# Performance work log

Measured on AMD Instinct MI355X. Metric: run time of the kernel, lower is better.

## Reference

```python
import jax, jax.numpy as jnp
import numpy as np

N_NODES = 100000
N_EDGES = 1600000
N_GRAPHS = 256
F_IN = 54


def setup_inputs() -> dict:
    key = jax.random.key(0)
    ks = jax.random.split(key, 16)
    x = jax.random.normal(ks[0], (N_NODES, F_IN), dtype=jnp.float32)
    edge_index = jax.random.randint(ks[1], (2, N_EDGES), 0, N_NODES, dtype=jnp.int32)
    batch = jnp.sort(jax.random.randint(ks[2], (N_NODES,), 0, N_GRAPHS, dtype=jnp.int32))

    def lin(k, fi, fo):
        kw, kb = jax.random.split(k)
        lim = 1.0 / np.sqrt(fi)
        W = jax.random.uniform(kw, (fi, fo), minval=-lim, maxval=lim, dtype=jnp.float32)
        b = jax.random.uniform(kb, (fo,), minval=-lim, maxval=lim, dtype=jnp.float32)
        return W, b

    W1, b1 = lin(ks[3], 54, 54)
    W2, b2 = lin(ks[4], 54, 108)
    W3, b3 = lin(ks[5], 108, 216)
    Wf1, bf1 = lin(ks[6], 216, 1024)
    Wf2, bf2 = lin(ks[7], 1024, 128)
    return {"x": x, "edge_index": edge_index, "batch": batch,
            "W1": W1, "b1": b1, "W2": W2, "b2": b2, "W3": W3, "b3": b3,
            "Wf1": Wf1, "bf1": bf1, "Wf2": Wf2, "bf2": bf2}


def _gcn_norm(edge_index, n):
    # add self-loops, symmetric degree normalization (PyG GCNConv default)
    loop = jnp.arange(n, dtype=edge_index.dtype)
    row = jnp.concatenate([edge_index[0], loop])
    col = jnp.concatenate([edge_index[1], loop])
    deg = jax.ops.segment_sum(jnp.ones_like(col, dtype=jnp.float32), col, num_segments=n)
    dinv = jnp.where(deg > 0, jax.lax.rsqrt(deg), 0.0)
    norm = dinv[row] * dinv[col]
    return row, col, norm


def _gcn_conv(x, row, col, norm, W, b, n):
    h = x @ W                                  # [N, Fout]
    msg = h[row] * norm[:, None]               # [E+N, Fout] gather + scale
    out = jax.ops.segment_sum(msg, col, num_segments=n)  # scatter-add
    return out + b


def reference(x, edge_index, batch, W1, b1, W2, b2, W3, b3, Wf1, bf1, Wf2, bf2):
    n = x.shape[0]
    row, col, norm = _gcn_norm(edge_index, n)
    h = jax.nn.relu(_gcn_conv(x, row, col, norm, W1, b1, n))
    h = jax.nn.relu(_gcn_conv(h, row, col, norm, W2, b2, n))
    h = jax.nn.relu(_gcn_conv(h, row, col, norm, W3, b3, n))
    # global mean pool per graph
    sums = jax.ops.segment_sum(h, batch, num_segments=N_GRAPHS)
    cnts = jax.ops.segment_sum(jnp.ones((n,), jnp.float32), batch, num_segments=N_GRAPHS)
    pooled = sums / jnp.maximum(cnts, 1.0)[:, None]   # [G, 216]
    g = jax.nn.relu(pooled @ Wf1 + bf1)               # dropout = identity (eval)
    return g @ Wf2 + bf2                              # [G, 128]
```

## Files before the change

### kernel.cpp

```cpp
#include <hip/hip_runtime.h>


typedef _Float16 f16;
typedef _Float16 f16x2 __attribute__((ext_vector_type(2)));
typedef _Float16 f16x8 __attribute__((ext_vector_type(8)));
typedef float f32x4 __attribute__((ext_vector_type(4)));

static __host__ __device__ inline int cdiv(int a, int b) { return (a + b - 1) / b; }

constexpr int BSPAN = 512;
constexpr int EPB   = 4096;
constexpr int EPT   = EPB / 256;

__device__ __forceinline__ void wpack_one(const float* W, f16* Wb, int K, int F,
                                          int KT, int idx) {
    int j = idx & 7;
    int lane = (idx >> 3) & 63;
    int fi = idx >> 9;
    int kt = fi % KT;
    int nt = fi / KT;
    int k = kt * 32 + (lane >> 4) * 8 + j;
    int nn = nt * 16 + (lane & 15);
    Wb[idx] = (k < K && nn < F) ? (f16)W[k * F + nn] : (f16)0.f;
}

__global__ __launch_bounds__(256) void k_init(
        const int* __restrict__ batch, int* __restrict__ start,
        float* __restrict__ psum, int* __restrict__ bktCnt, int* __restrict__ bktCur,
        const int* __restrict__ col,
        const float* __restrict__ W1, const float* __restrict__ W2,
        const float* __restrict__ W3, f16* __restrict__ w1b,
        f16* __restrict__ w2b, f16* __restrict__ w3b,
        int e, int nb, int n, int g) {
    __shared__ int hist[256];
    int t = threadIdx.x;
    int i = blockIdx.x * blockDim.x + t;
    hist[t] = 0;
    __syncthreads();
    int ebase = blockIdx.x * EPB;
#pragma unroll
    for (int j = 0; j < EPT; j++) {
        int idx = ebase + j * 256 + t;
        if (idx < e) atomicAdd(&hist[col[idx] >> 9], 1);
    }
    if (i < g * 216) psum[i] = 0.f;
    if (i < 256) bktCur[i] = 0;
    constexpr int T1 = 4 * 2 * 512;
    constexpr int T2 = 7 * 2 * 512;
    constexpr int T3 = 14 * 4 * 512;
    if (i < T1) wpack_one(W1, w1b, 54, 54, 2, i);
    else if (i < T1 + T2) wpack_one(W2, w2b, 54, 108, 2, i - T1);
    else if (i < T1 + T2 + T3) wpack_one(W3, w3b, 108, 216, 4, i - T1 - T2);
    if (i < n) {
        int b = batch[i];
        int bp = (i == 0) ? -1 : batch[i - 1];
        for (int gg = bp + 1; gg <= b; gg++) start[gg] = i;
        if (i == n - 1)
            for (int gg = b + 1; gg <= g; gg++) start[gg] = n;
    }
    __syncthreads();
    if (t < nb && hist[t] > 0) atomicAdd(&bktCnt[t], hist[t]);
}

__device__ __forceinline__ int scan256_ex(int* sbuf, int v, int t) {
    sbuf[t] = v;
    __syncthreads();
    for (int off = 1; off < 256; off <<= 1) {
        int x = sbuf[t];
        int y = (t >= off) ? sbuf[t - off] : 0;
        __syncthreads();
        sbuf[t] = x + y;
        __syncthreads();
    }
    return sbuf[t] - v;
}

__global__ __launch_bounds__(256) void k_bkt_part(const int* __restrict__ row,
                                                  const int* __restrict__ col,
                                                  const int* __restrict__ bktCnt,
                                                  int* bktCur, unsigned int* __restrict__ ebuf,
                                                  int e, int nb) {
    __shared__ int sbuf[256];
    __shared__ int hist[256];
    __shared__ int base[256];
    __shared__ int lcur[256];
    int t = threadIdx.x;
    int boff = scan256_ex(sbuf, (t < nb) ? bktCnt[t] : 0, t);
    hist[t] = 0; lcur[t] = 0;
    __syncthreads();
    int bs = blockIdx.x * EPB;
    unsigned int pk[EPT];
    int b[EPT];
#pragma unroll
    for (int j = 0; j < EPT; j++) {
        int idx = bs + j * 256 + t;
        if (idx < e) {
            int c = col[idx];
            pk[j] = ((unsigned int)(c & (BSPAN - 1)) << 17) | (unsigned int)row[idx];
            b[j] = c >> 9;
            atomicAdd(&hist[b[j]], 1);
        } else b[j] = -1;
    }
    __syncthreads();
    if (t < nb && hist[t] > 0) base[t] = boff + atomicAdd(&bktCur[t], hist[t]);
    __syncthreads();
#pragma unroll
    for (int j = 0; j < EPT; j++) {
        if (b[j] >= 0) {
            int lofs = atomicAdd(&lcur[b[j]], 1);
            ebuf[base[b[j]] + lofs] = pk[j];
        }
    }
}

__global__ __launch_bounds__(256) void k_bkt_build(const unsigned int* __restrict__ ebuf,
                                                   const int* __restrict__ bktCnt,
                                                   int* __restrict__ rowptr,
                                                   float* __restrict__ dinv,
                                                   int* __restrict__ eSrc,
                                                   int n, int nb) {
    __shared__ int sbuf[256];
    __shared__ int hist[BSPAN];
    __shared__ int cur[BSPAN];
    int t = threadIdx.x;
    int bkt = blockIdx.x;

    int boff_ex = scan256_ex(sbuf, (t < nb) ? bktCnt[t] : 0, t);
    __shared__ int boff_s, cnt_s;
    if (t == bkt) boff_s = boff_ex;
    if (t == 0) cnt_s = bktCnt[bkt];
    hist[t] = 0; hist[t + 256] = 0;
    __syncthreads();
    int es = boff_s, ee = boff_s + cnt_s;

    {
        int i = es + t;
        for (; i + 3 * 256 < ee; i += 4 * 256) {
            unsigned p0 = ebuf[i], p1 = ebuf[i + 256], p2 = ebuf[i + 512], p3 = ebuf[i + 768];
            atomicAdd(&hist[p0 >> 17], 1);
            atomicAdd(&hist[p1 >> 17], 1);
            atomicAdd(&hist[p2 >> 17], 1);
            atomicAdd(&hist[p3 >> 17], 1);
        }
        for (; i < ee; i += 256) atomicAdd(&hist[ebuf[i] >> 17], 1);
    }
    __syncthreads();

    int h0 = hist[2 * t], h1 = hist[2 * t + 1];
    __syncthreads();
    int ex = scan256_ex(sbuf, h0 + h1, t);
    int e0 = es + ex, e1 = e0 + h0;

    int node0 = bkt * BSPAN;
    int n0 = node0 + 2 * t, n1 = node0 + 2 * t + 1;
    if (n0 <= n) rowptr[n0] = e0;
    if (n1 <= n) rowptr[n1] = e1;
    if (n0 < n) dinv[n0] = rsqrtf((float)(h0 + 1));
    if (n1 < n) dinv[n1] = rsqrtf((float)(h1 + 1));
    cur[2 * t] = e0; cur[2 * t + 1] = e1;
    __syncthreads();

    {
        int i = es + t;
        for (; i + 3 * 256 < ee; i += 4 * 256) {
            unsigned p0 = ebuf[i], p1 = ebuf[i + 256], p2 = ebuf[i + 512], p3 = ebuf[i + 768];
            int s0 = atomicAdd(&cur[p0 >> 17], 1);
            int s1 = atomicAdd(&cur[p1 >> 17], 1);
            int s2 = atomicAdd(&cur[p2 >> 17], 1);
            int s3 = atomicAdd(&cur[p3 >> 17], 1);
            eSrc[s0] = (int)(p0 & 0x1FFFFu);
            eSrc[s1] = (int)(p1 & 0x1FFFFu);
            eSrc[s2] = (int)(p2 & 0x1FFFFu);
            eSrc[s3] = (int)(p3 & 0x1FFFFu);
        }
        for (; i < ee; i += 256) {
            unsigned int p = ebuf[i];
            int slot = atomicAdd(&cur[p >> 17], 1);
            eSrc[slot] = (int)(p & 0x1FFFFu);
        }
    }
}

template <int F, int RS>
__global__ void k_prescale(const float* __restrict__ x, const float* __restrict__ dinv,
                           f16* __restrict__ xs, int n) {
    constexpr int CH = F / 2;
    int idx = blockIdx.x * blockDim.x + threadIdx.x;
    if (idx >= n * CH) return;
    int node = idx / CH;
    int c = idx - node * CH;
    float d = dinv[node];
    float2 v = *reinterpret_cast<const float2*>(x + (long long)node * F + c * 2);
    f16x2 h;
    h[0] = (f16)(v.x * d);
    h[1] = (f16)(v.y * d);
    *reinterpret_cast<f16x2*>(xs + (long long)node * RS + c * 2) = h;
}

template <int F, int RS>
__global__ __launch_bounds__(256) void k_gatherw(
        const int* __restrict__ rowptr, const int* __restrict__ eSrc,
        const float* __restrict__ dinv, const f16* __restrict__ hs,
        f16* __restrict__ out, int n) {
    constexpr int CGN = RS / 8;
    constexpr int EPW = 64 / CGN;
    int wave = threadIdx.x >> 6;
    int lane = threadIdx.x & 63;
    int eslot = lane / CGN;
    int cg = lane & (CGN - 1);
    int node = blockIdx.x * 4 + wave;
    if (node >= n) return;
    int ch0 = cg * 8;
    int lim = F - ch0;
    if (lim > 8) lim = 8;
    if (lim < 0) lim = 0;

    int rs_ = rowptr[node], re = rowptr[node + 1];
    float di = dinv[node];
    int deg = re - rs_;
    int myidx = 0;
    if (lane < deg) myidx = eSrc[rs_ + lane];

    const f16x8* src = reinterpret_cast<const f16x8*>(hs);
    float acc[8];
#pragma unroll
    for (int j = 0; j < 8; j++) acc[j] = 0.f;

    if (eslot == 0) {
        f16x8 v = src[(long long)node * CGN + cg];
#pragma unroll
        for (int j = 0; j < 8; j++) acc[j] += (float)v[j];
    }

    int nfull = deg < 64 ? deg : 64;
    for (int base = 0; base < nfull; base += 8 * EPW) {
        int sidx[8];
#pragma unroll
        for (int u = 0; u < 8; u++) {
            int idx = base + u * EPW + eslot;
            sidx[u] = __shfl(myidx, idx < 63 ? idx : 63);
        }
        f16x8 v[8];
#pragma unroll
        for (int u = 0; u < 8; u++) {
            int idx = base + u * EPW + eslot;
            if (idx < nfull) v[u] = src[(long long)sidx[u] * CGN + cg];
        }
#pragma unroll
        for (int u = 0; u < 8; u++) {
            int idx = base + u * EPW + eslot;
            if (idx < nfull) {
#pragma unroll
                for (int j = 0; j < 8; j++) acc[j] += (float)v[u][j];
            }
        }
    }
    for (int e = rs_ + 64 + eslot; e < re; e += EPW) {
        int s = eSrc[e];
        f16x8 v = src[(long long)s * CGN + cg];
#pragma unroll
        for (int j = 0; j < 8; j++) acc[j] += (float)v[j];
    }

#pragma unroll
    for (int j = 0; j < 8; j++)
        if (j >= lim) acc[j] = 0.f;
#pragma unroll
    for (int m = CGN; m < 64; m <<= 1)
#pragma unroll
        for (int j = 0; j < 8; j++) acc[j] += __shfl_xor(acc[j], m);

    if (eslot == 0) {
        f16x8 o;
#pragma unroll
        for (int j = 0; j < 8; j++) o[j] = (f16)(acc[j] * di);
        *reinterpret_cast<f16x8*>(out + (long long)node * RS + ch0) = o;
    }
}

template <int F, int KTILES, int NTILES, int FOUT, int OSTR>
__global__ __launch_bounds__(256) void k_gcn_fused(
        const int* __restrict__ rowptr, const int* __restrict__ eSrc,
        const float* __restrict__ dinv, const f16* __restrict__ hs,
        const f16* __restrict__ Wb, const float* __restrict__ bias,
        f16* __restrict__ outh, int n) {
    constexpr int KPAD = KTILES * 32;
    constexpr int KP   = KPAD + 8;
    constexpr int CGN  = KPAD / 8;
    constexpr int EPH  = 32 / CGN;

    __shared__ __align__(16) f16 a_lds[64 * KP];

    int t = threadIdx.x;
    int node0 = blockIdx.x * 64;
    int w = t >> 6;
    int lane = t & 63;
    int half = lane >> 5;
    int l = lane & 31;
    int eslot = l / CGN;
    int cg = l & (CGN - 1);
    int ch0 = cg * 8;
    int lim = F - ch0;
    if (lim > 8) lim = 8;
    if (lim < 0) lim = 0;
    int lbase = half * 32;

    const f16x8* src = reinterpret_cast<const f16x8*>(hs);
    int nodeBase = node0 + w * 16;

    int rpIdx = nodeBase + (lane < 17 ? lane : 16);
    if (rpIdx > n) rpIdx = n;
    int rp = rowptr[rpIdx];
    int dvIdx = nodeBase + (lane < 16 ? lane : 15);
    if (dvIdx > n - 1) dvIdx = n - 1;
    float dvl = dinv[dvIdx];

    int rs_c = __shfl(rp, half);
    int re_c = __shfl(rp, 1 + half);
    int deg_c = re_c - rs_c;
    int my_c = 0;
    if (l < deg_c) my_c = eSrc[rs_c + l];
    f16x8 sv_c = {};
    if (eslot == 0 && nodeBase + half < n)
        sv_c = src[(long long)(nodeBase + half) * CGN + cg];

    for (int i = 0; i < 8; i++) {
        int node = nodeBase + 2 * i + half;
        int nfull = deg_c < 32 ? deg_c : 32;

        int sidx[8];
#pragma unroll
        for (int u = 0; u < 8; u++) {
            int idx = u * EPH + eslot;
            sidx[u] = __shfl(my_c, lbase + (idx < 31 ? idx : 31));
        }
        f16x8 v[8];
#pragma unroll
        for (int u = 0; u < 8; u++) {
            int idx = u * EPH + eslot;
            if (idx < nfull) v[u] = src[(long long)sidx[u] * CGN + cg];
        }

        int rs_n = 0, re_n = 0, deg_n = 0, my_n = 0;
        f16x8 sv_n = {};
        if (i < 7) {
            rs_n = __shfl(rp, 2 * i + 2 + half);
            re_n = __shfl(rp, 2 * i + 3 + half);
            deg_n = re_n - rs_n;
            if (l < deg_n) my_n = eSrc[rs_n + l];
            int node2 = nodeBase + 2 * i + 2 + half;
            if (eslot == 0 && node2 < n)
                sv_n = src[(long long)node2 * CGN + cg];
        }

        float acc[8];
#pragma unroll
        for (int j = 0; j < 8; j++) acc[j] = 0.f;
        if (eslot == 0) {
#pragma unroll
            for (int j = 0; j < 8; j++) acc[j] += (float)sv_c[j];
        }
#pragma unroll
        for (int u = 0; u < 8; u++) {
            int idx = u * EPH + eslot;
            if (idx < nfull) {
#pragma unroll
                for (int j = 0; j < 8; j++) acc[j] += (float)v[u][j];
            }
        }
        for (int e = rs_c + 32 + eslot; e < re_c; e += EPH) {
            int s = eSrc[e];
            f16x8 vv = src[(long long)s * CGN + cg];
#pragma unroll
            for (int j = 0; j < 8; j++) acc[j] += (float)vv[j];
        }

#pragma unroll
        for (int j = 0; j < 8; j++)
            if (j >= lim) acc[j] = 0.f;
#pragma unroll
        for (int m = CGN; m < 32; m <<= 1)
#pragma unroll
            for (int j = 0; j < 8; j++) acc[j] += __shfl_xor(acc[j], m);

        float di = (node < n) ? __shfl(dvl, 2 * i + half) : 0.f;
        if (eslot == 0) {
            f16x8 o;
#pragma unroll
            for (int j = 0; j < 8; j++) o[j] = (f16)(acc[j] * di);
            *reinterpret_cast<f16x8*>(&a_lds[(w * 16 + 2 * i + half) * KP + ch0]) = o;
        }
        rs_c = rs_n; re_c = re_n; deg_c = deg_n; my_c = my_n; sv_c = sv_n;
    }
    __syncthreads();

    int quad = lane >> 4;
    int col = lane & 15;

    f16x8 afr[KTILES];
#pragma unroll
    for (int kt = 0; kt < KTILES; kt++)
        afr[kt] = *reinterpret_cast<const f16x8*>(
            &a_lds[(16 * w + col) * KP + kt * 32 + quad * 8]);

    int nodeC = node0 + 16 * w + quad * 4;
    float dv[4];
#pragma unroll
    for (int r = 0; r < 4; r++) {
        int nd = nodeC + r;
        dv[r] = (nd < n) ? dinv[nd] : 0.f;
    }

    const f16x8* wb = reinterpret_cast<const f16x8*>(Wb);
#pragma unroll
    for (int nt = 0; nt < NTILES; nt++) {
        f16x8 bfr[KTILES];
#pragma unroll
        for (int kt = 0; kt < KTILES; kt++)
            bfr[kt] = wb[(nt * KTILES + kt) * 64 + lane];
        f32x4 acc = {0.f, 0.f, 0.f, 0.f};
#pragma unroll
        for (int kt = 0; kt < KTILES; kt++)
            acc = __builtin_amdgcn_mfma_f32_16x16x32_f16(afr[kt], bfr[kt], acc, 0, 0, 0);

        int ch = nt * 16 + col;
        if (ch < FOUT) {
            float bval = bias[ch];
#pragma unroll
            for (int r = 0; r < 4; r++) {
                int nd = nodeC + r;
                if (nd < n)
                    outh[(long long)nd * OSTR + ch] =
                        (f16)(fmaxf(acc[r] + bval, 0.f) * dv[r]);
            }
        }
    }
}

template <int KTILES, int NTILES, int K, int FOUT>
__global__ __launch_bounds__(256) void k_gemm_pool(
        const f16* __restrict__ in, const f16* __restrict__ Wb,
        const float* __restrict__ bias, const int* __restrict__ batch,
        float* __restrict__ psum, int n) {
    constexpr int KPAD = KTILES * 32;
    constexpr int KP   = KPAD + 8;
    constexpr int V8   = KPAD / 8;
    constexpr int NSLOT = 4;

    __shared__ f16 a_lds[64 * KP];
    __shared__ float psum_l[NSLOT * FOUT];

    int t = threadIdx.x;
    int node0 = blockIdx.x * 64;

    const f16x8* inp = reinterpret_cast<const f16x8*>(in);
    for (int f = t; f < 64 * V8; f += 256) {
        int node = f / V8;
        int v = f - node * V8;
        f16x8 val = {};
        if (node0 + node < n) val = inp[(long long)(node0 + node) * V8 + v];
        *reinterpret_cast<f16x8*>(&a_lds[node * KP + v * 8]) = val;
    }
    for (int i = t; i < NSLOT * FOUT; i += 256) psum_l[i] = 0.f;
    __syncthreads();

    int w = t >> 6;
    int lane = t & 63;
    int quad = lane >> 4;
    int col = lane & 15;

    f16x8 afr[KTILES];
#pragma unroll
    for (int kt = 0; kt < KTILES; kt++)
        afr[kt] = *reinterpret_cast<const f16x8*>(
            &a_lds[(16 * w + col) * KP + kt * 32 + quad * 8]);

    int nodeC = node0 + 16 * w + quad * 4;
    int gb[4];
#pragma unroll
    for (int r = 0; r < 4; r++) {
        int nd = nodeC + r;
        gb[r] = (nd < n) ? batch[nd] : -1;
    }
    int g0 = batch[node0];

    const f16x8* wb = reinterpret_cast<const f16x8*>(Wb);
#pragma unroll
    for (int nt = 0; nt < NTILES; nt++) {
        f16x8 bfr[KTILES];
#pragma unroll
        for (int kt = 0; kt < KTILES; kt++)
            bfr[kt] = wb[(nt * KTILES + kt) * 64 + lane];
        f32x4 acc = {0.f, 0.f, 0.f, 0.f};
#pragma unroll
        for (int kt = 0; kt < KTILES; kt++)
            acc = __builtin_amdgcn_mfma_f32_16x16x32_f16(afr[kt], bfr[kt], acc, 0, 0, 0);

        int ch = nt * 16 + col;
        if (ch < FOUT) {
            float bval = bias[ch];
            if (gb[0] == gb[3] && gb[0] >= 0) {
                float s = fmaxf(acc[0] + bval, 0.f) + fmaxf(acc[1] + bval, 0.f)
                        + fmaxf(acc[2] + bval, 0.f) + fmaxf(acc[3] + bval, 0.f);
                int slot = gb[0] - g0;
                if (slot < NSLOT) atomicAdd(&psum_l[slot * FOUT + ch], s);
                else atomicAdd(&psum[gb[0] * FOUT + ch], s);
            } else {
#pragma unroll
                for (int r = 0; r < 4; r++) {
                    if (gb[r] < 0) continue;
                    float v = fmaxf(acc[r] + bval, 0.f);
                    int slot = gb[r] - g0;
                    if (slot < NSLOT) atomicAdd(&psum_l[slot * FOUT + ch], v);
                    else atomicAdd(&psum[gb[r] * FOUT + ch], v);
                }
            }
        }
    }

    __syncthreads();
    int lastNode = node0 + 63;
    if (lastNode >= n) lastNode = n - 1;
    int nsl = batch[lastNode] - g0 + 1;
    if (nsl > NSLOT) nsl = NSLOT;
    for (int f = t; f < nsl * FOUT; f += 256) {
        float v = psum_l[f];
        if (v != 0.f) atomicAdd(&psum[(g0 + f / FOUT) * FOUT + (f % FOUT)], v);
    }
}

__global__ void k_fc1(const float* __restrict__ P, const int* __restrict__ start,
                      const float* __restrict__ W, const float* __restrict__ bias,
                      float* __restrict__ out) {
    int row = blockIdx.x >> 2;
    int o = (blockIdx.x & 3) * 256 + threadIdx.x;
    int cnt = start[row + 1] - start[row];
    float scale = 1.0f / fmaxf((float)cnt, 1.0f);
    __shared__ float prow[216];
    if (threadIdx.x < 216) prow[threadIdx.x] = P[row * 216 + threadIdx.x] * scale;
    __syncthreads();
    float acc = bias[o];
    for (int k = 0; k < 216; k++) acc += prow[k] * W[k * 1024 + o];
    out[row * 1024 + o] = fmaxf(acc, 0.f);
}
__global__ void k_fc2(const float* __restrict__ G, const float* __restrict__ W,
                      const float* __restrict__ bias, float* __restrict__ out) {
    int row = blockIdx.x;
    int o = threadIdx.x;
    __shared__ float grow[1024];
    for (int k = threadIdx.x; k < 1024; k += 128) grow[k] = G[row * 1024 + k];
    __syncthreads();
    float acc = bias[o];
    for (int k = 0; k < 1024; k++) acc += grow[k] * W[k * 128 + o];
    out[row * 128 + o] = acc;
}

extern "C" void kernel_launch(void* const* d_in, const int* in_sizes, int n_in,
                              void* d_out, int out_size, void* d_ws, size_t ws_size,
                              hipStream_t stream) {
    const float* x     = (const float*)d_in[0];
    const int*   ei    = (const int*)d_in[1];
    const int*   batch = (const int*)d_in[2];
    const float* W1  = (const float*)d_in[3];
    const float* b1  = (const float*)d_in[4];
    const float* W2  = (const float*)d_in[5];
    const float* b2  = (const float*)d_in[6];
    const float* W3  = (const float*)d_in[7];
    const float* b3  = (const float*)d_in[8];
    const float* Wf1 = (const float*)d_in[9];
    const float* bf1 = (const float*)d_in[10];
    const float* Wf2 = (const float*)d_in[11];
    const float* bf2 = (const float*)d_in[12];
    float* out = (float*)d_out;

    const int N = in_sizes[0] / 54;
    const int E = in_sizes[1] / 2;
    const int G = 256;
    const int* row = ei;
    const int* col = ei + E;
    const int NB = cdiv(N, BSPAN);
    const int NBLK_A = cdiv(E, EPB);

    char* ws = (char*)d_ws;
    size_t off = 0;
    auto carve = [&](size_t bytes) {
        void* p = ws + off;
        off += (bytes + 255) & ~(size_t)255;
        return p;
    };
    int*   rowptr  = (int*)carve((size_t)(N + 1) * 4);
    int*   bktCnt  = (int*)carve(256 * 4);
    int*   bktCur  = (int*)carve(256 * 4);
    int*   eSrc    = (int*)carve((size_t)E * 4);
    float* dinv    = (float*)carve((size_t)N * 4);
    f16*   xs      = (f16*)carve((size_t)N * 64 * 2);
    f16*   hsbuf   = (f16*)carve((size_t)N * 128 * 2);
    f16*   bufA    = (f16*)carve((size_t)N * 128 * 2);
    unsigned int* ebuf = (unsigned int*)carve((size_t)E * 4);
    float* psum    = (float*)carve((size_t)G * 216 * 4);
    float* gbuf    = (float*)carve((size_t)G * 1024 * 4);
    int*   start   = (int*)carve((size_t)(G + 1) * 4);
    f16*   w1b     = (f16*)carve((size_t)4 * 2 * 512 * 2);
    f16*   w2b     = (f16*)carve((size_t)7 * 2 * 512 * 2);
    f16*   w3b     = (f16*)carve((size_t)14 * 4 * 512 * 2);

    const int T = 256;
    hipMemsetAsync(bktCnt, 0, 256 * 4, stream);

    int gInit = cdiv(N, T) > NBLK_A ? cdiv(N, T) : NBLK_A;
    k_init<<<gInit, T, 0, stream>>>(batch, start, psum, bktCnt, bktCur, col,
                                    W1, W2, W3, w1b, w2b, w3b, E, NB, N, G);

    k_bkt_part<<<NBLK_A, 256, 0, stream>>>(row, col, bktCnt, bktCur, ebuf, E, NB);
    k_bkt_build<<<NB, 256, 0, stream>>>(ebuf, bktCnt, rowptr, dinv, eSrc, N, NB);

    k_prescale<54, 64><<<cdiv(N * 27, T), T, 0, stream>>>(x, dinv, xs, N);

    const int GB = cdiv(N, 64);

    k_gcn_fused<54, 2, 4, 54, 64><<<GB, 256, 0, stream>>>(
        rowptr, eSrc, dinv, xs, w1b, b1, hsbuf, N);

    k_gcn_fused<54, 2, 7, 108, 128><<<GB, 256, 0, stream>>>(
        rowptr, eSrc, dinv, hsbuf, w2b, b2, bufA, N);

    k_gatherw<108, 128><<<cdiv(N, 4), 256, 0, stream>>>(rowptr, eSrc, dinv, bufA, hsbuf, N);
    k_gemm_pool<4, 14, 108, 216><<<GB, 256, 0, stream>>>(
        hsbuf, w3b, b3, batch, psum, N);

    k_fc1<<<G * 4, T, 0, stream>>>(psum, start, Wf1, bf1, gbuf);
    k_fc2<<<G, 128, 0, stream>>>(gbuf, Wf2, bf2, out);
}
```

Measured before the change: 361.5 us.

## Gather two nodes per wave with deeper load batching; fuse FC layers

The layer-3 gather kernel now gives each half-wave (32 lanes) its own node, so eight nodes run per block. It issues up to 12 independent neighbour loads before accumulating, which raises memory-level parallelism for the average degree of about 17. The two FC kernels are merged into one kernel per graph that keeps the 1024-wide hidden vector in shared memory, removing a launch and the global round-trip. The fused FC runs only 256 blocks with more serial work per thread, and the gather uses more registers for the deeper batch.

```diff
diff --git a/kernel.cpp b/kernel.cpp
--- a/kernel.cpp
+++ b/kernel.cpp
@@ -198,64 +198,80 @@
 }
 
 template <int F, int RS>
-__global__ __launch_bounds__(256) void k_gatherw(
+__global__ __launch_bounds__(256) void k_gatherw2(
         const int* __restrict__ rowptr, const int* __restrict__ eSrc,
         const float* __restrict__ dinv, const f16* __restrict__ hs,
         f16* __restrict__ out, int n) {
     constexpr int CGN = RS / 8;
-    constexpr int EPW = 64 / CGN;
+    constexpr int EPH = 32 / CGN;
+    constexpr int DEPTH = 12;
     int wave = threadIdx.x >> 6;
     int lane = threadIdx.x & 63;
-    int eslot = lane / CGN;
-    int cg = lane & (CGN - 1);
-    int node = blockIdx.x * 4 + wave;
-    if (node >= n) return;
+    int half = lane >> 5;
+    int l = lane & 31;
+    int eslot = l / CGN;
+    int cg = l & (CGN - 1);
+    int lbase = half * 32;
+    int node = blockIdx.x * 8 + wave * 2 + half;
+    bool alive = node < n;
     int ch0 = cg * 8;
     int lim = F - ch0;
     if (lim > 8) lim = 8;
     if (lim < 0) lim = 0;
 
-    int rs_ = rowptr[node], re = rowptr[node + 1];
-    float di = dinv[node];
+    int rs_ = 0, re = 0;
+    float di = 0.f;
+    if (alive) {
+        rs_ = rowptr[node];
+        re = rowptr[node + 1];
+        di = dinv[node];
+    }
     int deg = re - rs_;
     int myidx = 0;
-    if (lane < deg) myidx = eSrc[rs_ + lane];
+    if (l < deg) myidx = eSrc[rs_ + l];
 
     const f16x8* src = reinterpret_cast<const f16x8*>(hs);
     float acc[8];
 #pragma unroll
     for (int j = 0; j < 8; j++) acc[j] = 0.f;
 
-    if (eslot == 0) {
+    if (alive && eslot == 0) {
         f16x8 v = src[(long long)node * CGN + cg];
 #pragma unroll
         for (int j = 0; j < 8; j++) acc[j] += (float)v[j];
     }
 
-    int nfull = deg < 64 ? deg : 64;
-    for (int base = 0; base < nfull; base += 8 * EPW) {
-        int sidx[8];
-#pragma unroll
-        for (int u = 0; u < 8; u++) {
-            int idx = base + u * EPW + eslot;
-            sidx[u] = __shfl(myidx, idx < 63 ? idx : 63);
-        }
-        f16x8 v[8];
-#pragma unroll
-        for (int u = 0; u < 8; u++) {
-            int idx = base + u * EPW + eslot;
-            if (idx < nfull) v[u] = src[(long long)sidx[u] * CGN + cg];
-        }
-#pragma unroll
-        for (int u = 0; u < 8; u++) {
-            int idx = base + u * EPW + eslot;
-            if (idx < nfull) {
+    int nfull = deg < 32 ? deg : 32;
+    int nbat = nfull < DEPTH * EPH ? nfull : DEPTH * EPH;
+    {
+        int sidx[DEPTH];
+#pragma unroll
+        for (int u = 0; u < DEPTH; u++) {
+            int idx = u * EPH + eslot;
+            sidx[u] = __shfl(myidx, lbase + (idx < 31 ? idx : 31));
+        }
+        f16x8 v[DEPTH];
+#pragma unroll
+        for (int u = 0; u < DEPTH; u++) {
+            int idx = u * EPH + eslot;
+            if (idx < nbat) v[u] = src[(long long)sidx[u] * CGN + cg];
+        }
+#pragma unroll
+        for (int u = 0; u < DEPTH; u++) {
+            int idx = u * EPH + eslot;
+            if (idx < nbat) {
 #pragma unroll
                 for (int j = 0; j < 8; j++) acc[j] += (float)v[u][j];
             }
         }
     }
-    for (int e = rs_ + 64 + eslot; e < re; e += EPW) {
+    for (int idx = DEPTH * EPH + eslot; idx < nfull; idx += EPH) {
+        int s = __shfl(myidx, lbase + idx);
+        f16x8 v = src[(long long)s * CGN + cg];
+#pragma unroll
+        for (int j = 0; j < 8; j++) acc[j] += (float)v[j];
+    }
+    for (int e = rs_ + 32 + eslot; e < re; e += EPH) {
         int s = eSrc[e];
         f16x8 v = src[(long long)s * CGN + cg];
 #pragma unroll
@@ -266,11 +282,11 @@
     for (int j = 0; j < 8; j++)
         if (j >= lim) acc[j] = 0.f;
 #pragma unroll
-    for (int m = CGN; m < 64; m <<= 1)
+    for (int m = CGN; m < 32; m <<= 1)
 #pragma unroll
         for (int j = 0; j < 8; j++) acc[j] += __shfl_xor(acc[j], m);
 
-    if (eslot == 0) {
+    if (alive && eslot == 0) {
         f16x8 o;
 #pragma unroll
         for (int j = 0; j < 8; j++) o[j] = (f16)(acc[j] * di);
@@ -529,30 +545,36 @@
     }
 }
 
-__global__ void k_fc1(const float* __restrict__ P, const int* __restrict__ start,
-                      const float* __restrict__ W, const float* __restrict__ bias,
-                      float* __restrict__ out) {
-    int row = blockIdx.x >> 2;
-    int o = (blockIdx.x & 3) * 256 + threadIdx.x;
+__global__ __launch_bounds__(256) void k_fc(const float* __restrict__ P,
+                                            const int* __restrict__ start,
+                                            const float* __restrict__ Wf1,
+                                            const float* __restrict__ bf1,
+                                            const float* __restrict__ Wf2,
+                                            const float* __restrict__ bf2,
+                                            float* __restrict__ out) {
+    int row = blockIdx.x;
+    int t = threadIdx.x;
+    __shared__ float prow[216];
+    __shared__ float g[1024];
+    __shared__ float part[256];
     int cnt = start[row + 1] - start[row];
     float scale = 1.0f / fmaxf((float)cnt, 1.0f);
-    __shared__ float prow[216];
-    if (threadIdx.x < 216) prow[threadIdx.x] = P[row * 216 + threadIdx.x] * scale;
-    __syncthreads();
-    float acc = bias[o];
-    for (int k = 0; k < 216; k++) acc += prow[k] * W[k * 1024 + o];
-    out[row * 1024 + o] = fmaxf(acc, 0.f);
-}
-__global__ void k_fc2(const float* __restrict__ G, const float* __restrict__ W,
-                      const float* __restrict__ bias, float* __restrict__ out) {
-    int row = blockIdx.x;
-    int o = threadIdx.x;
-    __shared__ float grow[1024];
-    for (int k = threadIdx.x; k < 1024; k += 128) grow[k] = G[row * 1024 + k];
-    __syncthreads();
-    float acc = bias[o];
-    for (int k = 0; k < 1024; k++) acc += grow[k] * W[k * 128 + o];
-    out[row * 128 + o] = acc;
+    if (t < 216) prow[t] = P[row * 216 + t] * scale;
+    __syncthreads();
+#pragma unroll
+    for (int p = 0; p < 4; p++) {
+        int o = t + 256 * p;
+        float acc = bf1[o];
+        for (int k = 0; k < 216; k++) acc += prow[k] * Wf1[k * 1024 + o];
+        g[o] = fmaxf(acc, 0.f);
+    }
+    __syncthreads();
+    int o = t & 127, h = t >> 7;
+    float acc = 0.f;
+    for (int k = h * 512; k < h * 512 + 512; k++) acc += g[k] * Wf2[k * 128 + o];
+    part[t] = acc;
+    __syncthreads();
+    if (t < 128) out[row * 128 + t] = part[t] + part[t + 128] + bf2[t];
 }
 
 extern "C" void kernel_launch(void* const* d_in, const int* in_sizes, int n_in,
@@ -598,7 +620,6 @@
     f16*   bufA    = (f16*)carve((size_t)N * 128 * 2);
     unsigned int* ebuf = (unsigned int*)carve((size_t)E * 4);
     float* psum    = (float*)carve((size_t)G * 216 * 4);
-    float* gbuf    = (float*)carve((size_t)G * 1024 * 4);
     int*   start   = (int*)carve((size_t)(G + 1) * 4);
     f16*   w1b     = (f16*)carve((size_t)4 * 2 * 512 * 2);
     f16*   w2b     = (f16*)carve((size_t)7 * 2 * 512 * 2);
@@ -624,10 +645,9 @@
     k_gcn_fused<54, 2, 7, 108, 128><<<GB, 256, 0, stream>>>(
         rowptr, eSrc, dinv, hsbuf, w2b, b2, bufA, N);
 
-    k_gatherw<108, 128><<<cdiv(N, 4), 256, 0, stream>>>(rowptr, eSrc, dinv, bufA, hsbuf, N);
+    k_gatherw2<108, 128><<<cdiv(N, 8), 256, 0, stream>>>(rowptr, eSrc, dinv, bufA, hsbuf, N);
     k_gemm_pool<4, 14, 108, 216><<<GB, 256, 0, stream>>>(
         hsbuf, w3b, b3, batch, psum, N);
 
-    k_fc1<<<G * 4, T, 0, stream>>>(psum, start, Wf1, bf1, gbuf);
-    k_fc2<<<G, 128, 0, stream>>>(gbuf, Wf2, bf2, out);
-}
+    k_fc<<<G, T, 0, stream>>>(psum, start, Wf1, bf1, Wf2, bf2, out);
+}
```

New measurement: 489.6 us. 1.35x slower.
